# Performance work log

Hardware: AMD Instinct MI355X
Metric: run time of the kernel (lower is better)

## Reference

```python
import jax, jax.numpy as jnp
import numpy as np

N = 100000


def seg_mean(feat, src, dst, n):
    # gather at src, scatter-mean at dst (PyG mean aggr: 0 for isolated nodes)
    s = jax.ops.segment_sum(feat[src], dst, num_segments=n)
    cnt = jax.ops.segment_sum(jnp.ones((src.shape[0],), feat.dtype), dst, num_segments=n)
    return s / jnp.maximum(cnt, 1.0)[:, None]


def setup_inputs() -> dict:
    key = jax.random.key(0)
    ks = jax.random.split(key, 8)
    d_in, d_h = 64, 32
    E = 1_250_000
    inp = {
        "x": jax.random.normal(ks[0], (N, d_in), jnp.float32),
        "W1_pos": jax.random.normal(ks[1], (2 * d_in, d_h), jnp.float32) * 0.05,
        "b1_pos": jnp.zeros((d_h,), jnp.float32),
        "W1_neg": jax.random.normal(ks[2], (2 * d_in, d_h), jnp.float32) * 0.05,
        "b1_neg": jnp.zeros((d_h,), jnp.float32),
        "W2_pos": jax.random.normal(ks[3], (3 * d_h, d_h), jnp.float32) * 0.05,
        "b2_pos": jnp.zeros((d_h,), jnp.float32),
        "W2_neg": jax.random.normal(ks[4], (3 * d_h, d_h), jnp.float32) * 0.05,
        "b2_neg": jnp.zeros((d_h,), jnp.float32),
        "pos_edge_index": jax.random.randint(ks[5], (2, E), 0, N, jnp.int64),
        "neg_edge_index": jax.random.randint(ks[6], (2, E), 0, N, jnp.int64),
    }
    return inp


def reference(x, W1_pos, b1_pos, W1_neg, b1_neg, W2_pos, b2_pos, W2_neg, b2_neg,
              pos_edge_index, neg_edge_index):
    ps, pd = pos_edge_index[0], pos_edge_index[1]
    ns, nd = neg_edge_index[0], neg_edge_index[1]
    n = x.shape[0]

    # --- layer 1 (first_aggr=True) ---
    ap = seg_mean(x, ps, pd, n)          # [N, 64]
    an = seg_mean(x, ns, nd, n)
    out_p = jnp.concatenate([ap, x], -1) @ W1_pos + b1_pos   # [N, 32]
    out_n = jnp.concatenate([an, x], -1) @ W1_neg + b1_neg
    z = jnp.tanh(jnp.concatenate([out_p, out_n], -1))        # [N, 64]

    # --- layer 2 (first_aggr=False) ---
    d_h = out_p.shape[-1]
    zp, zn = z[:, :d_h], z[:, d_h:]
    out_p = jnp.concatenate([seg_mean(zp, ps, pd, n), seg_mean(zn, ns, nd, n), zp], -1) @ W2_pos + b2_pos
    out_n = jnp.concatenate([seg_mean(zn, ps, pd, n), seg_mean(zp, ns, nd, n), zn], -1) @ W2_neg + b2_neg
    z = jnp.tanh(jnp.concatenate([out_p, out_n], -1))
    return z
```

## Files before the change

kernel.cpp:

```cpp
#include <hip/hip_runtime.h>
#include <math.h>


typedef _Float16 h4 __attribute__((ext_vector_type(4)));
typedef _Float16 h8 __attribute__((ext_vector_type(8)));
typedef float f32x4 __attribute__((ext_vector_type(4)));

__device__ inline h8 shflx8(h8 v, int m) {
    int4 i = __builtin_bit_cast(int4, v);
    i.x = __shfl_xor(i.x, m);
    i.y = __shfl_xor(i.y, m);
    i.z = __shfl_xor(i.z, m);
    i.w = __shfl_xor(i.w, m);
    return __builtin_bit_cast(h8, i);
}

__device__ inline float fast_tanh(float v) {
    float e = __expf(2.0f * v);
    return 1.0f - 2.0f / (e + 1.0f);
}


#define BSHIFT 9
#define BSIZE  512
#define NBMAX  512
#define NREP   8
#define RCAP   1024
#define CAP    (NREP * RCAP)
#define MAXPER 1280


__device__ inline float b1map(const float* W1p, const float* W1n, int k, int c)
{
    if (c < 32) {
        if (k < 64)   return W1p[k * 32 + c];
        if (k >= 128) return W1p[(k - 64) * 32 + c];
        return 0.0f;
    } else {
        int cn = c - 32;
        if (k >= 64)  return W1n[(k - 64) * 32 + cn];
        return 0.0f;
    }
}

__device__ inline float b2map(const float* W2p, const float* W2n, int k, int c)
{
    if (c < 32) {
        if (k < 32)               return W2p[k * 32 + c];
        if (k >= 96 && k < 128)   return W2p[(k - 96 + 32) * 32 + c];
        if (k >= 128 && k < 160)  return W2p[(k - 128 + 64) * 32 + c];
        return 0.0f;
    } else {
        int cn = c - 32;
        if (k >= 32 && k < 64)    return W2n[(k - 32) * 32 + cn];
        if (k >= 64 && k < 96)    return W2n[(k - 64 + 32) * 32 + cn];
        if (k >= 160)             return W2n[(k - 160 + 64) * 32 + cn];
        return 0.0f;
    }
}


__global__ void __launch_bounds__(256) mega_k(
    const int* __restrict__ pos, const int* __restrict__ neg,
    int* __restrict__ pcntR, unsigned* __restrict__ ebuf,
    int E, int n, int nb, int bblocks,
    const float4* __restrict__ x, h4* __restrict__ xh, int n4, int cvtBlocks,
    const float* __restrict__ W1p, const float* __restrict__ W1n,
    const float* __restrict__ W2p, const float* __restrict__ W2n,
    _Float16* __restrict__ Bpack)
{
    int tid = threadIdx.x;
    int bid = blockIdx.x;

    if (bid >= bblocks) {
        int cb = bid - bblocks;
        if (cb < cvtBlocks) {
            int gs = cvtBlocks * 256;
            for (int i = cb * 256 + tid; i < n4; i += gs) {
                float4 v = x[i];
                h4 o = { (_Float16)v.x, (_Float16)v.y, (_Float16)v.z, (_Float16)v.w };
                xh[i] = o;
            }
        } else {
            int slot = (cb - cvtBlocks) * 256 + tid;
            if (slot < 2 * 24 * 64) {
                int mat  = slot / (24 * 64);
                int rem  = slot % (24 * 64);
                int fg   = rem / 64;
                int lane = rem % 64;
                int kk = fg >> 2, nt = fg & 3;
                int g = lane >> 4, m = lane & 15;
                _Float16* dst = Bpack + (size_t)slot * 8;
                int c = nt * 16 + m;
                #pragma unroll
                for (int j = 0; j < 8; ++j) {
                    int k = kk * 32 + g * 8 + j;
                    float v = mat ? b2map(W2p, W2n, k, c) : b1map(W1p, W1n, k, c);
                    dst[j] = (_Float16)v;
                }
            }
        }
        return;
    }

    __shared__ int cnt[NBMAX], gbase[NBMAX];
    __shared__ unsigned erec[MAXPER];
    __shared__ unsigned short ep[MAXPER];
    int rep = bid & (NREP - 1);
    int per = (2 * E + bblocks - 1) / bblocks;
    int e0 = bid * per;
    int e1 = min(e0 + per, 2 * E);
    int cntloc = e1 - e0;

    for (int i = tid; i < nb; i += 256) cnt[i] = 0;
    __syncthreads();

    for (int e = e0 + tid; e < e1; e += 256) {
        int nd, sr;
        if (e < E) { nd = pos[E + e];                 sr = pos[e]; }
        else       { int ee = e - E; nd = n + neg[E + ee]; sr = neg[ee]; }
        int p = nd >> BSHIFT;
        int li = e - e0;
        erec[li] = ((unsigned)(nd & (BSIZE - 1)) << 17) | (unsigned)sr;
        ep[li] = (unsigned short)p;
        atomicAdd(&cnt[p], 1);
    }
    __syncthreads();
    for (int i = tid; i < nb; i += 256) {
        int c = cnt[i];
        gbase[i] = c ? atomicAdd(&pcntR[rep * NBMAX + i], c) : 0;
        cnt[i] = 0;
    }
    __syncthreads();
    for (int li = tid; li < cntloc; li += 256) {
        int p = ep[li];
        int r = gbase[p] + atomicAdd(&cnt[p], 1);
        if (r < RCAP)
            ebuf[(size_t)p * CAP + rep * RCAP + r] = erec[li];
    }
}

__global__ void __launch_bounds__(1024) scatter_k(
    const unsigned* __restrict__ ebuf, const int* __restrict__ pcntR,
    int* __restrict__ cur, int* __restrict__ col, int n, int nb)
{
    __shared__ int lcnt[BSIZE], lbase[BSIZE], sc[256], bb[NBMAX], crp[NREP];
    __shared__ int lcol[CAP];
    int p = blockIdx.x;
    int tid = threadIdx.x;
    int n2 = 2 * n;
    int lo = p << BSHIFT;
    int nn = min(BSIZE, n2 - lo);
    const unsigned* bbuf = ebuf + (size_t)p * CAP;

    if (tid < NREP) crp[tid] = min(pcntR[tid * NBMAX + p], RCAP);

    {
        int a0 = 0, a1 = 0, s = 0;
        if (tid < 256) {
            #pragma unroll
            for (int r = 0; r < NREP; ++r) {
                if (2 * tid     < nb) a0 += min(pcntR[r * NBMAX + 2 * tid],     RCAP);
                if (2 * tid + 1 < nb) a1 += min(pcntR[r * NBMAX + 2 * tid + 1], RCAP);
            }
            s = a0 + a1;
            sc[tid] = s;
        }
        __syncthreads();
        for (int off = 1; off < 256; off <<= 1) {
            int t = (tid < 256 && tid >= off) ? sc[tid - off] : 0;
            __syncthreads();
            if (tid < 256) sc[tid] += t;
            __syncthreads();
        }
        if (tid < 256) {
            int excl = sc[tid] - s;
            bb[2 * tid]     = excl;
            bb[2 * tid + 1] = excl + a0;
        }
    }

    for (int i = tid; i < BSIZE; i += 1024) lcnt[i] = 0;
    __syncthreads();
    int cnttot = crp[0] + crp[1] + crp[2] + crp[3] +
                 crp[4] + crp[5] + crp[6] + crp[7];
    #pragma unroll
    for (int r = 0; r < NREP; ++r) {
        int c = crp[r];
        const unsigned* buf = bbuf + r * RCAP;
        for (int i = tid; i < c; i += 1024)
            atomicAdd(&lcnt[buf[i] >> 17], 1);
    }
    __syncthreads();
    {
        int a0 = 0, a1 = 0, s = 0;
        if (tid < 256) {
            a0 = lcnt[2 * tid]; a1 = lcnt[2 * tid + 1];
            s = a0 + a1;
            sc[tid] = s;
        }
        __syncthreads();
        for (int off = 1; off < 256; off <<= 1) {
            int t = (tid < 256 && tid >= off) ? sc[tid - off] : 0;
            __syncthreads();
            if (tid < 256) sc[tid] += t;
            __syncthreads();
        }
        if (tid < 256) {
            int excl = sc[tid] - s;
            lbase[2 * tid]     = excl;
            lbase[2 * tid + 1] = excl + a0;
        }
    }
    __syncthreads();
    int gb = bb[p];
    for (int i = tid; i < nn; i += 1024)
        cur[lo + i] = gb + lbase[i] + lcnt[i];
    __syncthreads();
    #pragma unroll
    for (int r = 0; r < NREP; ++r) {
        int c = crp[r];
        const unsigned* buf = bbuf + r * RCAP;
        for (int i = tid; i < c; i += 1024) {
            unsigned v = buf[i];
            int slot = atomicAdd(&lbase[v >> 17], 1);
            lcol[slot] = (int)(v & 0x1FFFFu);
        }
    }
    __syncthreads();
    for (int t = tid; t < cnttot; t += 1024)
        col[gb + t] = lcol[t];
}


__global__ void __launch_bounds__(256) agg_k(
    const h8* __restrict__ feat8,
    const int* __restrict__ cur, const int* __restrict__ col,
    h8* __restrict__ ag8, int n)
{
    int tid = threadIdx.x;
    int wave = tid >> 6, lane = tid & 63;
    int s = lane >> 2, f = lane & 3;
    int list = s >> 3;
    int sub = s & 7;

    int stride = gridDim.x * 4;
    for (int node = blockIdx.x * 4 + wave; node < n; node += stride) {
        int idx = list ? n + node : node;
        int r0 = idx ? cur[idx - 1] : 0;
        int r1 = cur[idx];

        h8 acc0 = {}, acc1 = {};
        #pragma unroll 2
        for (int it = r0 + sub; it < r1; it += 8) {
            unsigned srcb = (unsigned)col[it] * 8;
            acc0 = acc0 + feat8[srcb + f];
            acc1 = acc1 + feat8[srcb + 4 + f];
        }
        acc0 = acc0 + shflx8(acc0, 4);
        acc1 = acc1 + shflx8(acc1, 4);
        acc0 = acc0 + shflx8(acc0, 8);
        acc1 = acc1 + shflx8(acc1, 8);
        acc0 = acc0 + shflx8(acc0, 16);
        acc1 = acc1 + shflx8(acc1, 16);
        _Float16 inv = (_Float16)(1.0f / (float)max(r1 - r0, 1));
        h8 iv = { inv, inv, inv, inv, inv, inv, inv, inv };
        if (sub == 0) {
            ag8[(unsigned)(node * 16 + list * 8 + f)]     = acc0 * iv;
            ag8[(unsigned)(node * 16 + list * 8 + 4 + f)] = acc1 * iv;
        }
    }
}


#define ROWP 200

__global__ void __launch_bounds__(256) gemm_k(
    const h8* __restrict__ ag8, const h8* __restrict__ feat8,
    const h8* __restrict__ Bp,
    const float* __restrict__ bp, const float* __restrict__ bn,
    float* __restrict__ outf, _Float16* __restrict__ outh,
    int f32out, int n)
{
    __shared__ _Float16 A_lds[64 * ROWP];
    int tid = threadIdx.x;
    int base = blockIdx.x * 64;

    for (int ch = tid; ch < 64 * 24; ch += 256) {
        int r = ch / 24, p = ch % 24;
        int row = min(base + r, n - 1);
        h8 v = (p < 16) ? ag8[(size_t)row * 16 + p]
                        : feat8[(size_t)row * 8 + (p - 16)];
        *(h8*)&A_lds[r * ROWP + p * 8] = v;
    }
    __syncthreads();

    int w = tid >> 6, lane = tid & 63;
    int m = lane & 15, g = lane >> 4;

    h8 a[6];
    #pragma unroll
    for (int kk = 0; kk < 6; ++kk)
        a[kk] = *(const h8*)&A_lds[(w * 16 + m) * ROWP + kk * 32 + g * 8];

    #pragma unroll
    for (int nt = 0; nt < 4; ++nt) {
        f32x4 acc = { 0.f, 0.f, 0.f, 0.f };
        #pragma unroll
        for (int kk = 0; kk < 6; ++kk) {
            h8 b = Bp[(kk * 4 + nt) * 64 + lane];
            acc = __builtin_amdgcn_mfma_f32_16x16x32_f16(a[kk], b, acc, 0, 0, 0);
        }
        int colc = nt * 16 + m;
        float bias = (colc < 32) ? bp[colc] : bn[colc - 32];
        #pragma unroll
        for (int reg = 0; reg < 4; ++reg) {
            int node = base + w * 16 + g * 4 + reg;
            if (node < n) {
                float val = fast_tanh(acc[reg] + bias);
                if (f32out) outf[(size_t)node * 64 + colc] = val;
                else        outh[(size_t)node * 64 + colc] = (_Float16)val;
            }
        }
    }
}

extern "C" void kernel_launch(void* const* d_in, const int* in_sizes, int n_in,
                              void* d_out, int out_size, void* d_ws, size_t ws_size,
                              hipStream_t stream)
{
    const float* x   = (const float*)d_in[0];
    const float* W1p = (const float*)d_in[1];
    const float* b1p = (const float*)d_in[2];
    const float* W1n = (const float*)d_in[3];
    const float* b1n = (const float*)d_in[4];
    const float* W2p = (const float*)d_in[5];
    const float* b2p = (const float*)d_in[6];
    const float* W2n = (const float*)d_in[7];
    const float* b2n = (const float*)d_in[8];
    const int*   pos = (const int*)d_in[9];
    const int*   neg = (const int*)d_in[10];

    int n = in_sizes[0] / 64;
    int E = in_sizes[9] / 2;
    int n2 = 2 * n;
    int nb = (n2 + BSIZE - 1) / BSIZE;

    int*      pcntR = (int*)d_ws;
    int*      cur   = pcntR + NREP * NBMAX;
    int*      col   = cur + n2;
    _Float16* Bpack = (_Float16*)(col + 2 * (size_t)E);
    _Float16* xh    = Bpack + 2 * 24 * 64 * 8;
    unsigned* ebuf  = (unsigned*)(xh + (size_t)n * 64);
    _Float16* zh    = (_Float16*)ebuf;
    h8*       ag8   = (h8*)d_out;

    hipMemsetAsync(pcntR, 0, NREP * NBMAX * sizeof(int), stream);

    int bblocks = 2048;
    int n4 = n * 16;
    int cvtBlocks = 512;

    mega_k<<<bblocks + cvtBlocks + 12, 256, 0, stream>>>(
        pos, neg, pcntR, ebuf, E, n, nb, bblocks,
        (const float4*)x, (h4*)xh, n4, cvtBlocks,
        W1p, W1n, W2p, W2n, Bpack);

    scatter_k<<<nb, 1024, 0, stream>>>(ebuf, pcntR, cur, col, n, nb);

    int ablocks = 2048;
    int gblocks = (n + 63) / 64;

    agg_k <<<ablocks, 256, 0, stream>>>((const h8*)xh, cur, col, ag8, n);
    gemm_k<<<gblocks, 256, 0, stream>>>(ag8, (const h8*)xh, (const h8*)Bpack,
                                        b1p, b1n, nullptr, zh, 0, n);

    agg_k <<<ablocks, 256, 0, stream>>>((const h8*)zh, cur, col, ag8, n);
    gemm_k<<<gblocks, 256, 0, stream>>>(ag8, (const h8*)zh,
                                        (const h8*)(Bpack + 24 * 64 * 8),
                                        b2p, b2n, (float*)d_out, nullptr, 1, n);
}
```

Measured before the change: 264.4 us.

## Locally sort edge records by bucket before global write; remap gemm node rows

The bucketing phase now runs with 512 blocks, each handling four times as many edges. Each block prefix-sums its per-bucket counts, sorts its edge records by bucket in shared memory, and then writes them to the global bucket buffers in contiguous runs. Previously each edge went straight to global memory at a scattered address, and the sorted write is meant to make those stores more coalesced. The gemm kernel also gets a new node-to-block mapping, with a few extra blocks launched to cover the remapped range. The larger shared arrays (about 50KB) lower occupancy, and fewer blocks reduce parallelism in the bucketing phase.

```diff
diff --git a/kernel.cpp b/kernel.cpp
--- a/kernel.cpp
+++ b/kernel.cpp
@@ -27,7 +27,7 @@
 #define NREP   8
 #define RCAP   1024
 #define CAP    (NREP * RCAP)
-#define MAXPER 1280
+#define MAXPER 4992
 
 
 __device__ inline float b1map(const float* W1p, const float* W1n, int k, int c)
@@ -103,9 +103,9 @@
         return;
     }
 
-    __shared__ int cnt[NBMAX], gbase[NBMAX];
-    __shared__ unsigned erec[MAXPER];
-    __shared__ unsigned short ep[MAXPER];
+    __shared__ int cnt[NBMAX], gbase[NBMAX], lofs[NBMAX], sc2[256];
+    __shared__ unsigned erec[MAXPER], sorted[MAXPER];
+    __shared__ unsigned short ep[MAXPER], pd[MAXPER];
     int rep = bid & (NREP - 1);
     int per = (2 * E + bblocks - 1) / bblocks;
     int e0 = bid * per;
@@ -129,14 +129,39 @@
     for (int i = tid; i < nb; i += 256) {
         int c = cnt[i];
         gbase[i] = c ? atomicAdd(&pcntR[rep * NBMAX + i], c) : 0;
-        cnt[i] = 0;
-    }
+    }
+    {
+        int a0 = (2 * tid     < nb) ? cnt[2 * tid]     : 0;
+        int a1 = (2 * tid + 1 < nb) ? cnt[2 * tid + 1] : 0;
+        int s = a0 + a1;
+        sc2[tid] = s;
+        __syncthreads();
+        for (int off = 1; off < 256; off <<= 1) {
+            int t = (tid >= off) ? sc2[tid - off] : 0;
+            __syncthreads();
+            sc2[tid] += t;
+            __syncthreads();
+        }
+        int excl = sc2[tid] - s;
+        if (2 * tid     < nb) lofs[2 * tid]     = excl;
+        if (2 * tid + 1 < nb) lofs[2 * tid + 1] = excl + a0;
+    }
+    __syncthreads();
+    for (int i = tid; i < nb; i += 256) cnt[i] = 0;
     __syncthreads();
     for (int li = tid; li < cntloc; li += 256) {
         int p = ep[li];
-        int r = gbase[p] + atomicAdd(&cnt[p], 1);
-        if (r < RCAP)
-            ebuf[(size_t)p * CAP + rep * RCAP + r] = erec[li];
+        int r = atomicAdd(&cnt[p], 1);
+        int idx = lofs[p] + r;
+        sorted[idx] = erec[li];
+        pd[idx] = (unsigned short)p;
+    }
+    __syncthreads();
+    for (int t = tid; t < cntloc; t += 256) {
+        int p = pd[t];
+        int g = gbase[p] + (t - lofs[p]);
+        if (g < RCAP)
+            ebuf[(size_t)p * CAP + rep * RCAP + g] = sorted[t];
     }
 }
 
@@ -275,6 +300,10 @@
 
 #define ROWP 200
 
+__device__ inline int nmap(int g, int r) {
+    return 32 * (16 * (g >> 3) + (r >> 2)) + 4 * (g & 7) + (r & 3);
+}
+
 __global__ void __launch_bounds__(256) gemm_k(
     const h8* __restrict__ ag8, const h8* __restrict__ feat8,
     const h8* __restrict__ Bp,
@@ -284,11 +313,11 @@
 {
     __shared__ _Float16 A_lds[64 * ROWP];
     int tid = threadIdx.x;
-    int base = blockIdx.x * 64;
+    int bid = blockIdx.x;
 
     for (int ch = tid; ch < 64 * 24; ch += 256) {
         int r = ch / 24, p = ch % 24;
-        int row = min(base + r, n - 1);
+        int row = min(nmap(bid, r), n - 1);
         h8 v = (p < 16) ? ag8[(size_t)row * 16 + p]
                         : feat8[(size_t)row * 8 + (p - 16)];
         *(h8*)&A_lds[r * ROWP + p * 8] = v;
@@ -315,7 +344,7 @@
         float bias = (colc < 32) ? bp[colc] : bn[colc - 32];
         #pragma unroll
         for (int reg = 0; reg < 4; ++reg) {
-            int node = base + w * 16 + g * 4 + reg;
+            int node = nmap(bid, w * 16 + g * 4 + reg);
             if (node < n) {
                 float val = fast_tanh(acc[reg] + bias);
                 if (f32out) outf[(size_t)node * 64 + colc] = val;
@@ -357,7 +386,7 @@
 
     hipMemsetAsync(pcntR, 0, NREP * NBMAX * sizeof(int), stream);
 
-    int bblocks = 2048;
+    int bblocks = 512;
     int n4 = n * 16;
     int cvtBlocks = 512;
 
@@ -369,7 +398,7 @@
     scatter_k<<<nb, 1024, 0, stream>>>(ebuf, pcntR, cur, col, n, nb);
 
     int ablocks = 2048;
-    int gblocks = (n + 63) / 64;
+    int gblocks = (n + 63) / 64 + 5;
 
     agg_k <<<ablocks, 256, 0, stream>>>((const h8*)xh, cur, col, ag8, n);
     gemm_k<<<gblocks, 256, 0, stream>>>(ag8, (const h8*)xh, (const h8*)Bpack,
```

New measurement: 262.6 us. No clear change (-0.7%).
